# Kernel tuning notes

Hardware: AMD Instinct MI355X
Metric: run time of the kernel (lower is better)

The kernel has to match this reference:

```python
import math
import jax, jax.numpy as jnp
import numpy as np

B, S, H, NH = 4, 2048, 1024, 16
HD = H // NH  # 64


def _rope_cos_sin(seq_len, dim, base=10000.0):
    # freqs[j] = base^(-2j/dim), angles = outer(t, freqs)
    inv = 1.0 / (base ** (jnp.arange(0, dim, 2, dtype=jnp.float32) / dim))
    t = jnp.arange(seq_len, dtype=jnp.float32)
    ang = jnp.outer(t, inv)  # (S, dim//2)
    return jnp.cos(ang), jnp.sin(ang)


def _apply_rope(x, cos, sin):
    # x: (B, S, NH, HD); pairs are (x[2i], x[2i+1]) per torch view_as_complex on reshape(..., -1, 2)
    xr = x.reshape(*x.shape[:-1], HD // 2, 2)
    x0, x1 = xr[..., 0], xr[..., 1]
    c = cos[None, :, None, :]  # (1, S, 1, HD//2)
    s = sin[None, :, None, :]
    o0 = x0 * c - x1 * s
    o1 = x0 * s + x1 * c
    return jnp.stack([o0, o1], axis=-1).reshape(x.shape)


def setup_inputs() -> dict:
    key = jax.random.key(0)
    ks = jax.random.split(key, 5)
    scale = 1.0 / math.sqrt(H)
    return {
        "x": jax.random.normal(ks[0], (B, S, H), dtype=jnp.float32),
        "wq": jax.random.normal(ks[1], (H, H), dtype=jnp.float32) * scale,
        "wk": jax.random.normal(ks[2], (H, H), dtype=jnp.float32) * scale,
        "wv": jax.random.normal(ks[3], (H, H), dtype=jnp.float32) * scale,
        "wo": jax.random.normal(ks[4], (H, H), dtype=jnp.float32) * scale,
        "attention_mask": jnp.ones((B, S), dtype=jnp.int32),
    }


def reference(x, wq, wk, wv, wo, attention_mask):
    # Linear(bias=False): y = x @ W.T with W shape (out, in)
    q = jnp.einsum('bsh,oh->bso', x, wq).reshape(B, S, NH, HD)
    k = jnp.einsum('bsh,oh->bso', x, wk).reshape(B, S, NH, HD)
    v = jnp.einsum('bsh,oh->bso', x, wv).reshape(B, S, NH, HD)
    cos, sin = _rope_cos_sin(S, HD)
    q = _apply_rope(q, cos, sin)
    k = _apply_rope(k, cos, sin)
    # scores: (B, NH, S, S)
    scores = jnp.einsum('bqhd,bkhd->bhqk', q, k) / math.sqrt(HD)
    mask = attention_mask[:, None, None, :]  # (B,1,1,S)
    scores = jnp.where(mask == 0, -jnp.inf, scores)
    attn = jax.nn.softmax(scores, axis=-1)
    # attn_dropout: eval mode / p=0 -> identity
    out = jnp.einsum('bhqk,bkhd->bqhd', attn, v).reshape(B, S, H)
    return jnp.einsum('bsh,oh->bso', out, wo)
```

## Files before the change

kernel.cpp:

```cpp
#include <hip/hip_runtime.h>
#include <hip/hip_bf16.h>

#define B_   4
#define S_   2048
#define H_   1024
#define NH_  16
#define HD_  64
#define M_   8192
#define K_   1024

using bf16x8 = __bf16 __attribute__((ext_vector_type(8)));
using f32x4  = float __attribute__((ext_vector_type(4)));
using f32x16 = float __attribute__((ext_vector_type(16)));

__device__ inline f32x4 mfma16(bf16x8 a, bf16x8 b, f32x4 c) {
    return __builtin_amdgcn_mfma_f32_16x16x32_bf16(a, b, c, 0, 0, 0);
}
__device__ inline f32x16 mfma32(bf16x8 a, bf16x8 b, f32x16 c) {
    return __builtin_amdgcn_mfma_f32_32x32x16_bf16(a, b, c, 0, 0, 0);
}

__device__ inline unsigned short f2bf(float f) {
    __hip_bfloat16 h = __float2bfloat16(f);
    return *reinterpret_cast<unsigned short*>(&h);
}

__device__ inline unsigned cvt_pk_bf16(float lo, float hi) {
    unsigned r;
    asm("v_cvt_pk_bf16_f32 %0, %1, %2" : "=v"(r) : "v"(lo), "v"(hi));
    return r;
}

__device__ inline void perm32swap(unsigned &a, unsigned &b) {
    asm("v_permlane32_swap_b32 %0, %1" : "+v"(a), "+v"(b));
}

__device__ inline void gload_lds16(const unsigned short* g, unsigned short* l) {
    __builtin_amdgcn_global_load_lds(
        (const __attribute__((address_space(1))) void*)g,
        (__attribute__((address_space(3))) void*)l, 16, 0, 0);
}

#define EXP2F(x) __builtin_amdgcn_exp2f(x)


__global__ __launch_bounds__(256) void prep_convert(
    const float* __restrict__ x,  const float* __restrict__ wq,
    const float* __restrict__ wk, const float* __restrict__ wv,
    const float* __restrict__ wo, unsigned short* __restrict__ ws)
{
    size_t u = (size_t)blockIdx.x * 256 + threadIdx.x;
    const float* src; unsigned short* dst; size_t off;
    if (u < 2097152)      { src = x;  dst = ws;            off = u * 4; }
    else if (u < 2359296) { src = wq; dst = ws + 8388608;  off = (u - 2097152) * 4; }
    else if (u < 2621440) { src = wk; dst = ws + 9437184;  off = (u - 2359296) * 4; }
    else if (u < 2883584) { src = wv; dst = ws + 10485760; off = (u - 2621440) * 4; }
    else                  { src = wo; dst = ws + 11534336; off = (u - 2883584) * 4; }
    float4 v = *reinterpret_cast<const float4*>(src + off);
    ushort4 o;
    o.x = f2bf(v.x); o.y = f2bf(v.y); o.z = f2bf(v.z); o.w = f2bf(v.w);
    *reinterpret_cast<ushort4*>(dst + off) = o;
}

__global__ __launch_bounds__(256) void rope_table(
    float* __restrict__ cosb, float* __restrict__ sinb,
    const int* __restrict__ mask, float* __restrict__ biasb)
{
    int idx = blockIdx.x * 256 + threadIdx.x;
    int pos = idx >> 5, i = idx & 31;
    float inv = expf(-(float)(2 * i) * (9.210340371976184f / 64.0f));
    float ang = (float)pos * inv;
    cosb[idx] = cosf(ang);
    sinb[idx] = sinf(ang);
    if (idx < B_ * S_)
        biasb[idx] = mask[idx] ? -12.0f : -__builtin_inff();
}

template<int EPI>
__global__ __launch_bounds__(256) void gemm_bt(
    const unsigned short* __restrict__ A,
    const unsigned short* __restrict__ W,
    void* __restrict__ outp,
    const float* __restrict__ cosb, const float* __restrict__ sinb,
    float scale)
{
    __shared__ alignas(16) unsigned short Al[128 * 64];
    __shared__ alignas(16) unsigned short Bl[128 * 64];

    const int t = threadIdx.x;
    const int l = t & 63;
    const int w = t >> 6;
    const int lane_r = l & 15, lane_g = l >> 4;
    const int bn = blockIdx.x, bm = blockIdx.y;
    const size_t rowbase = (size_t)bm * 128;
    const int colbase = bn * 128;
    const int wm = (w >> 1) * 64, wn = (w & 1) * 64;

    const int glrow  = l >> 3;
    const int glslot = (l & 7) ^ glrow;

    f32x4 zero4 = {0.f, 0.f, 0.f, 0.f};
    f32x4 acc[4][4];
#pragma unroll
    for (int a = 0; a < 4; a++)
#pragma unroll
        for (int b2 = 0; b2 < 4; b2++) acc[a][b2] = zero4;

    for (int k0 = 0; k0 < K_; k0 += 64) {
#pragma unroll
        for (int i = 0; i < 4; i++) {
            int rbase = i * 32 + w * 8;
            int row = rbase + glrow;
            gload_lds16(A + (rowbase + row) * K_ + k0 + glslot * 8, &Al[rbase * 64]);
            gload_lds16(W + (size_t)(colbase + row) * K_ + k0 + glslot * 8, &Bl[rbase * 64]);
        }
        __syncthreads();

        bf16x8 af[4][2], bfr[4][2];
#pragma unroll
        for (int mt = 0; mt < 4; mt++)
#pragma unroll
            for (int kk = 0; kk < 2; kk++) {
                int rowa = wm + mt * 16 + lane_r;
                int offa = (rowa * 128 + kk * 64 + lane_g * 16) ^ ((rowa & 7) << 4);
                af[mt][kk] = *reinterpret_cast<const bf16x8*>((const char*)Al + offa);
                int rowb = wn + mt * 16 + lane_r;
                int offb = (rowb * 128 + kk * 64 + lane_g * 16) ^ ((rowb & 7) << 4);
                bfr[mt][kk] = *reinterpret_cast<const bf16x8*>((const char*)Bl + offb);
            }
#pragma unroll
        for (int mt = 0; mt < 4; mt++)
#pragma unroll
            for (int nt = 0; nt < 4; nt++) {
                acc[mt][nt] = mfma16(af[mt][0], bfr[nt][0], acc[mt][nt]);
                acc[mt][nt] = mfma16(af[mt][1], bfr[nt][1], acc[mt][nt]);
            }
        __syncthreads();
    }

#pragma unroll
    for (int mt = 0; mt < 4; mt++) {
#pragma unroll
        for (int nt = 0; nt < 4; nt++) {
            if constexpr (EPI == 2) {
                float* out = (float*)outp;
#pragma unroll
                for (int i = 0; i < 4; i++) {
                    size_t r = rowbase + wm + mt * 16 + lane_g * 4 + i;
                    int n = colbase + wn + nt * 16 + lane_r;
                    out[r * 1024 + n] = acc[mt][nt][i];
                }
            } else if constexpr (EPI == 0) {
                unsigned short* out = (unsigned short*)outp;
#pragma unroll
                for (int i = 0; i < 4; i++) {
                    size_t r = rowbase + wm + mt * 16 + lane_g * 4 + i;
                    int n = colbase + wn + nt * 16 + lane_r;
                    int b   = (int)(r >> 11);
                    int pos = (int)(r & 2047);
                    int h = n >> 6, d = n & 63;
                    float cv = cosb[pos * 32 + (d >> 1)];
                    float sv = sinb[pos * 32 + (d >> 1)];
                    float val = acc[mt][nt][i];
                    float partner = __shfl_xor(val, 1);
                    float o = (d & 1) ? (partner * sv + val * cv)
                                      : (val * cv - partner * sv);
                    o *= scale;
                    out[(((size_t)(b * NH_ + h)) * S_ + pos) * 64 + d] = f2bf(o);
                }
            } else {
                unsigned short* out = (unsigned short*)outp;
                size_t rr = rowbase + wm + mt * 16 + lane_g * 4;
                int n = colbase + wn + nt * 16 + lane_r;
                int b   = (int)(rr >> 11);
                int pos = (int)(rr & 2047);
                int h = n >> 6, d = n & 63;
                ushort4 o;
                o.x = f2bf(acc[mt][nt][0]); o.y = f2bf(acc[mt][nt][1]);
                o.z = f2bf(acc[mt][nt][2]); o.w = f2bf(acc[mt][nt][3]);
                *reinterpret_cast<ushort4*>(
                    out + (((size_t)(b * NH_ + h)) * 64 + d) * S_ + pos) = o;
            }
        }
    }
}

__global__ __launch_bounds__(256) void attn_fwd(
    const unsigned short* __restrict__ qb, const unsigned short* __restrict__ kb,
    const unsigned short* __restrict__ vt, const float* __restrict__ biasb,
    unsigned short* __restrict__ ao)
{
    __shared__ alignas(16) unsigned short Kl[2][64 * 64];
    __shared__ alignas(16) unsigned short Vl[2][64 * 64];

    const int bid = blockIdx.x;
    const int xcd = bid & 7, idx = bid >> 3;
    const int bh = xcd * 8 + (idx >> 4);
    const int qt = idx & 15;
    const int b = bh >> 4, h = bh & 15;

    const int t = threadIdx.x, l = t & 63, w = t >> 6;
    const int lr = l & 31;
    const int hi = l >> 5;
    const int row8 = lr & 7;

    const unsigned short* qp = qb + (size_t)bh * S_ * 64;
    const unsigned short* kp = kb + (size_t)bh * S_ * 64;
    const unsigned short* vp = vt + (size_t)bh * 64 * S_;
    const float* bp = biasb + (size_t)b * S_;

    bf16x8 qf[4];
    {
        int qrow = qt * 128 + w * 32 + lr;
#pragma unroll
        for (int ks = 0; ks < 4; ks++)
            qf[ks] = *reinterpret_cast<const bf16x8*>(
                qp + (size_t)qrow * 64 + ks * 16 + hi * 8);
    }

    f32x16 oacc[2];
#pragma unroll
    for (int r = 0; r < 16; r++) { oacc[0][r] = 0.f; oacc[1][r] = 0.f; }
    float lsum = 0.f;

    const int grr = l >> 3;
    const int gss = ((l & 7) ^ grr) * 8;

#define STAGE(bi, kt)                                                          \
    {                                                                          \
        _Pragma("unroll")                                                      \
        for (int c = 0; c < 2; c++) {                                          \
            int rbase = w * 16 + c * 8;                                        \
            gload_lds16(kp + (size_t)((kt) * 64 + rbase + grr) * 64 + gss,     \
                        &Kl[bi][rbase * 64]);                                  \
            gload_lds16(vp + (size_t)(rbase + grr) * S_ + (kt) * 64 + gss,     \
                        &Vl[bi][rbase * 64]);                                  \
        }                                                                      \
    }

    STAGE(0, 0)

    for (int kt = 0; kt < 32; kt++) {
        const int cur = kt & 1;
        __syncthreads();
        if (kt < 31) STAGE(cur ^ 1, kt + 1)

        f32x16 sacc[2];
#pragma unroll
        for (int T = 0; T < 2; T++)
#pragma unroll
            for (int g = 0; g < 4; g++) {
                float4 bv = *reinterpret_cast<const float4*>(
                    bp + kt * 64 + T * 32 + g * 8 + hi * 4);
                sacc[T][g * 4 + 0] = bv.x; sacc[T][g * 4 + 1] = bv.y;
                sacc[T][g * 4 + 2] = bv.z; sacc[T][g * 4 + 3] = bv.w;
            }

        __builtin_amdgcn_s_setprio(1);
#pragma unroll
        for (int T = 0; T < 2; T++) {
            int rowb = (32 * T + lr) * 128;
#pragma unroll
            for (int ks = 0; ks < 4; ks++) {
                bf16x8 kf = *reinterpret_cast<const bf16x8*>(
                    (const char*)Kl[cur] + rowb + (((2 * ks + hi) ^ row8) << 4));
                sacc[T] = mfma32(kf, qf[ks], sacc[T]);
            }
        }
        __builtin_amdgcn_s_setprio(0);

        unsigned u[2][8];
        float r0 = 0.f, r1 = 0.f, r2 = 0.f, r3 = 0.f;
#pragma unroll
        for (int T = 0; T < 2; T++) {
            float p[16];
#pragma unroll
            for (int r = 0; r < 16; r++) p[r] = EXP2F(sacc[T][r]);
#pragma unroll
            for (int r = 0; r < 16; r += 4) {
                r0 += p[r]; r1 += p[r + 1]; r2 += p[r + 2]; r3 += p[r + 3];
            }
#pragma unroll
            for (int bq = 0; bq < 4; bq++) {
                u[T][bq * 2 + 0] = cvt_pk_bf16(p[bq * 4 + 0], p[bq * 4 + 1]);
                u[T][bq * 2 + 1] = cvt_pk_bf16(p[bq * 4 + 2], p[bq * 4 + 3]);
            }
        }
        lsum += (r0 + r1) + (r2 + r3);

        bf16x8 pa[4];
#pragma unroll
        for (int ks = 0; ks < 4; ks++) {
            int T = ks >> 1, e = ks & 1;
            unsigned a0 = u[T][4 * e + 0], b0 = u[T][4 * e + 2];
            unsigned a1 = u[T][4 * e + 1], b1 = u[T][4 * e + 3];
            perm32swap(a0, b0);
            perm32swap(a1, b1);
            unsigned q4[4] = {a0, a1, b0, b1};
            pa[ks] = *reinterpret_cast<const bf16x8*>(q4);
        }

        __builtin_amdgcn_s_setprio(1);
#pragma unroll
        for (int dt = 0; dt < 2; dt++) {
            int rowb = (32 * dt + lr) * 128;
#pragma unroll
            for (int ks = 0; ks < 4; ks++) {
                bf16x8 vf = *reinterpret_cast<const bf16x8*>(
                    (const char*)Vl[cur] + rowb + (((2 * ks + hi) ^ row8) << 4));
                oacc[dt] = mfma32(vf, pa[ks], oacc[dt]);
            }
        }
        __builtin_amdgcn_s_setprio(0);
    }
#undef STAGE

    lsum += __shfl_xor(lsum, 32);
    float rl = 1.0f / lsum;
    size_t obase = ((size_t)(b * S_) + qt * 128 + w * 32 + lr) * 1024 + h * 64;
#pragma unroll
    for (int dt = 0; dt < 2; dt++)
#pragma unroll
        for (int g = 0; g < 4; g++) {
            uint2 o;
            o.x = cvt_pk_bf16(oacc[dt][g * 4 + 0] * rl, oacc[dt][g * 4 + 1] * rl);
            o.y = cvt_pk_bf16(oacc[dt][g * 4 + 2] * rl, oacc[dt][g * 4 + 3] * rl);
            *reinterpret_cast<uint2*>(ao + obase + 32 * dt + 8 * g + 4 * hi) = o;
        }
}

extern "C" void kernel_launch(void* const* d_in, const int* in_sizes, int n_in,
                              void* d_out, int out_size, void* d_ws, size_t ws_size,
                              hipStream_t stream)
{
    const float* x  = (const float*)d_in[0];
    const float* wq = (const float*)d_in[1];
    const float* wk = (const float*)d_in[2];
    const float* wv = (const float*)d_in[3];
    const float* wo = (const float*)d_in[4];
    const int* mask = (const int*)d_in[5];

    unsigned short* ws   = (unsigned short*)d_ws;
    unsigned short* xb   = ws;
    unsigned short* wqb  = ws + 8388608;
    unsigned short* wkb  = ws + 9437184;
    unsigned short* wvb  = ws + 10485760;
    unsigned short* wob  = ws + 11534336;
    unsigned short* qbuf = ws + 12582912;
    unsigned short* kbuf = ws + 20971520;
    unsigned short* vtb  = ws + 29360128;
    float* cosb  = (float*)(ws + 37748736);
    float* sinb  = cosb + 65536;
    float* biasb = sinb + 65536;
    unsigned short* aob = xb;

    prep_convert<<<12288, 256, 0, stream>>>(x, wq, wk, wv, wo, ws);
    rope_table<<<256, 256, 0, stream>>>(cosb, sinb, mask, biasb);

    dim3 ggrid(8, 64);
    gemm_bt<0><<<ggrid, 256, 0, stream>>>(xb, wqb, qbuf, cosb, sinb, 0.18033688089184827f);
    gemm_bt<0><<<ggrid, 256, 0, stream>>>(xb, wkb, kbuf, cosb, sinb, 1.0f);
    gemm_bt<1><<<ggrid, 256, 0, stream>>>(xb, wvb, vtb, nullptr, nullptr, 1.0f);

    attn_fwd<<<1024, 256, 0, stream>>>(qbuf, kbuf, vtb, biasb, aob);

    gemm_bt<2><<<ggrid, 256, 0, stream>>>(aob, wob, d_out, nullptr, nullptr, 1.0f);
}
```

Measured before the change: 229.3 us.

## Fuse QKV projections into one GEMM launch and double query rows per attention block

The three Q/K/V projection GEMMs become a single launch over the contiguous concatenated weight buffer, with the output target chosen per column block. The attention kernel now gives each wave two 32-row query sub-tiles that share every K/V tile loaded into LDS, halving the grid and doubling K/V reuse. Register pressure in attention rises (launch bounds set to 2 blocks per SM), and fewer blocks may reduce latency hiding.

```diff
diff --git a/kernel.cpp b/kernel.cpp
--- a/kernel.cpp
+++ b/kernel.cpp
@@ -76,13 +76,12 @@
         biasb[idx] = mask[idx] ? -12.0f : -__builtin_inff();
 }
 
-template<int EPI>
-__global__ __launch_bounds__(256) void gemm_bt(
+__global__ __launch_bounds__(256) void gemm_qkv(
     const unsigned short* __restrict__ A,
     const unsigned short* __restrict__ W,
-    void* __restrict__ outp,
-    const float* __restrict__ cosb, const float* __restrict__ sinb,
-    float scale)
+    unsigned short* __restrict__ qbuf, unsigned short* __restrict__ kbuf,
+    unsigned short* __restrict__ vtb,
+    const float* __restrict__ cosb, const float* __restrict__ sinb)
 {
     __shared__ alignas(16) unsigned short Al[128 * 64];
     __shared__ alignas(16) unsigned short Bl[128 * 64];
@@ -95,6 +94,8 @@
     const size_t rowbase = (size_t)bm * 128;
     const int colbase = bn * 128;
     const int wm = (w >> 1) * 64, wn = (w & 1) * 64;
+    const int which = colbase >> 10;
+    const float scale = (which == 0) ? 0.18033688089184827f : 1.0f;
 
     const int glrow  = l >> 3;
     const int glslot = (l & 7) ^ glrow;
@@ -142,20 +143,12 @@
     for (int mt = 0; mt < 4; mt++) {
 #pragma unroll
         for (int nt = 0; nt < 4; nt++) {
-            if constexpr (EPI == 2) {
-                float* out = (float*)outp;
+            if (which <= 1) {
+                unsigned short* out = which ? kbuf : qbuf;
 #pragma unroll
                 for (int i = 0; i < 4; i++) {
                     size_t r = rowbase + wm + mt * 16 + lane_g * 4 + i;
-                    int n = colbase + wn + nt * 16 + lane_r;
-                    out[r * 1024 + n] = acc[mt][nt][i];
-                }
-            } else if constexpr (EPI == 0) {
-                unsigned short* out = (unsigned short*)outp;
-#pragma unroll
-                for (int i = 0; i < 4; i++) {
-                    size_t r = rowbase + wm + mt * 16 + lane_g * 4 + i;
-                    int n = colbase + wn + nt * 16 + lane_r;
+                    int n = (colbase & 1023) + wn + nt * 16 + lane_r;
                     int b   = (int)(r >> 11);
                     int pos = (int)(r & 2047);
                     int h = n >> 6, d = n & 63;
@@ -169,9 +162,9 @@
                     out[(((size_t)(b * NH_ + h)) * S_ + pos) * 64 + d] = f2bf(o);
                 }
             } else {
-                unsigned short* out = (unsigned short*)outp;
+                unsigned short* out = vtb;
                 size_t rr = rowbase + wm + mt * 16 + lane_g * 4;
-                int n = colbase + wn + nt * 16 + lane_r;
+                int n = (colbase & 1023) + wn + nt * 16 + lane_r;
                 int b   = (int)(rr >> 11);
                 int pos = (int)(rr & 2047);
                 int h = n >> 6, d = n & 63;
@@ -185,7 +178,78 @@
     }
 }
 
-__global__ __launch_bounds__(256) void attn_fwd(
+__global__ __launch_bounds__(256) void gemm_wo(
+    const unsigned short* __restrict__ A,
+    const unsigned short* __restrict__ W,
+    float* __restrict__ out)
+{
+    __shared__ alignas(16) unsigned short Al[128 * 64];
+    __shared__ alignas(16) unsigned short Bl[128 * 64];
+
+    const int t = threadIdx.x;
+    const int l = t & 63;
+    const int w = t >> 6;
+    const int lane_r = l & 15, lane_g = l >> 4;
+    const int bn = blockIdx.x, bm = blockIdx.y;
+    const size_t rowbase = (size_t)bm * 128;
+    const int colbase = bn * 128;
+    const int wm = (w >> 1) * 64, wn = (w & 1) * 64;
+
+    const int glrow  = l >> 3;
+    const int glslot = (l & 7) ^ glrow;
+
+    f32x4 zero4 = {0.f, 0.f, 0.f, 0.f};
+    f32x4 acc[4][4];
+#pragma unroll
+    for (int a = 0; a < 4; a++)
+#pragma unroll
+        for (int b2 = 0; b2 < 4; b2++) acc[a][b2] = zero4;
+
+    for (int k0 = 0; k0 < K_; k0 += 64) {
+#pragma unroll
+        for (int i = 0; i < 4; i++) {
+            int rbase = i * 32 + w * 8;
+            int row = rbase + glrow;
+            gload_lds16(A + (rowbase + row) * K_ + k0 + glslot * 8, &Al[rbase * 64]);
+            gload_lds16(W + (size_t)(colbase + row) * K_ + k0 + glslot * 8, &Bl[rbase * 64]);
+        }
+        __syncthreads();
+
+        bf16x8 af[4][2], bfr[4][2];
+#pragma unroll
+        for (int mt = 0; mt < 4; mt++)
+#pragma unroll
+            for (int kk = 0; kk < 2; kk++) {
+                int rowa = wm + mt * 16 + lane_r;
+                int offa = (rowa * 128 + kk * 64 + lane_g * 16) ^ ((rowa & 7) << 4);
+                af[mt][kk] = *reinterpret_cast<const bf16x8*>((const char*)Al + offa);
+                int rowb = wn + mt * 16 + lane_r;
+                int offb = (rowb * 128 + kk * 64 + lane_g * 16) ^ ((rowb & 7) << 4);
+                bfr[mt][kk] = *reinterpret_cast<const bf16x8*>((const char*)Bl + offb);
+            }
+#pragma unroll
+        for (int mt = 0; mt < 4; mt++)
+#pragma unroll
+            for (int nt = 0; nt < 4; nt++) {
+                acc[mt][nt] = mfma16(af[mt][0], bfr[nt][0], acc[mt][nt]);
+                acc[mt][nt] = mfma16(af[mt][1], bfr[nt][1], acc[mt][nt]);
+            }
+        __syncthreads();
+    }
+
+#pragma unroll
+    for (int mt = 0; mt < 4; mt++)
+#pragma unroll
+        for (int nt = 0; nt < 4; nt++)
+#pragma unroll
+            for (int i = 0; i < 4; i++) {
+                size_t r = rowbase + wm + mt * 16 + lane_g * 4 + i;
+                int n = colbase + wn + nt * 16 + lane_r;
+                out[r * 1024 + n] = acc[mt][nt][i];
+            }
+}
+
+__global__ __launch_bounds__(256, 2) void attn_fwd(
     const unsigned short* __restrict__ qb, const unsigned short* __restrict__ kb,
     const unsigned short* __restrict__ vt, const float* __restrict__ biasb,
     unsigned short* __restrict__ ao)
@@ -195,8 +259,8 @@
 
     const int bid = blockIdx.x;
     const int xcd = bid & 7, idx = bid >> 3;
-    const int bh = xcd * 8 + (idx >> 4);
-    const int qt = idx & 15;
+    const int bh = xcd * 8 + (idx >> 3);
+    const int qt = idx & 7;
     const int b = bh >> 4, h = bh & 15;
 
     const int t = threadIdx.x, l = t & 63, w = t >> 6;
@@ -209,19 +273,22 @@
     const unsigned short* vp = vt + (size_t)bh * 64 * S_;
     const float* bp = biasb + (size_t)b * S_;
 
-    bf16x8 qf[4];
-    {
-        int qrow = qt * 128 + w * 32 + lr;
+    bf16x8 qf[2][4];
+#pragma unroll
+    for (int qbk = 0; qbk < 2; qbk++) {
+        int qrow = qt * 256 + w * 64 + qbk * 32 + lr;
 #pragma unroll
         for (int ks = 0; ks < 4; ks++)
-            qf[ks] = *reinterpret_cast<const bf16x8*>(
+            qf[qbk][ks] = *reinterpret_cast<const bf16x8*>(
                 qp + (size_t)qrow * 64 + ks * 16 + hi * 8);
     }
 
-    f32x16 oacc[2];
-#pragma unroll
-    for (int r = 0; r < 16; r++) { oacc[0][r] = 0.f; oacc[1][r] = 0.f; }
-    float lsum = 0.f;
+    f32x16 oacc[2][2];
+#pragma unroll
+    for (int qbk = 0; qbk < 2; qbk++)
+#pragma unroll
+        for (int r = 0; r < 16; r++) { oacc[qbk][0][r] = 0.f; oacc[qbk][1][r] = 0.f; }
+    float lsum[2] = {0.f, 0.f};
 
     const int grr = l >> 3;
     const int gss = ((l & 7) ^ grr) * 8;
@@ -245,16 +312,18 @@
         __syncthreads();
         if (kt < 31) STAGE(cur ^ 1, kt + 1)
 
-        f32x16 sacc[2];
-#pragma unroll
-        for (int T = 0; T < 2; T++)
+        f32x16 sacc[2][2];
+#pragma unroll
+        for (int T = 0; T < 2; T++) {
 #pragma unroll
             for (int g = 0; g < 4; g++) {
                 float4 bv = *reinterpret_cast<const float4*>(
                     bp + kt * 64 + T * 32 + g * 8 + hi * 4);
-                sacc[T][g * 4 + 0] = bv.x; sacc[T][g * 4 + 1] = bv.y;
-                sacc[T][g * 4 + 2] = bv.z; sacc[T][g * 4 + 3] = bv.w;
-            }
+                sacc[0][T][g * 4 + 0] = bv.x; sacc[0][T][g * 4 + 1] = bv.y;
+                sacc[0][T][g * 4 + 2] = bv.z; sacc[0][T][g * 4 + 3] = bv.w;
+            }
+            sacc[1][T] = sacc[0][T];
+        }
 
         __builtin_amdgcn_s_setprio(1);
 #pragma unroll
@@ -264,40 +333,43 @@
             for (int ks = 0; ks < 4; ks++) {
                 bf16x8 kf = *reinterpret_cast<const bf16x8*>(
                     (const char*)Kl[cur] + rowb + (((2 * ks + hi) ^ row8) << 4));
-                sacc[T] = mfma32(kf, qf[ks], sacc[T]);
+                sacc[0][T] = mfma32(kf, qf[0][ks], sacc[0][T]);
+                sacc[1][T] = mfma32(kf, qf[1][ks], sacc[1][T]);
             }
         }
         __builtin_amdgcn_s_setprio(0);
 
-        unsigned u[2][8];
-        float r0 = 0.f, r1 = 0.f, r2 = 0.f, r3 = 0.f;
-#pragma unroll
-        for (int T = 0; T < 2; T++) {
-            float p[16];
-#pragma unroll
-            for (int r = 0; r < 16; r++) p[r] = EXP2F(sacc[T][r]);
-#pragma unroll
-            for (int r = 0; r < 16; r += 4) {
-                r0 += p[r]; r1 += p[r + 1]; r2 += p[r + 2]; r3 += p[r + 3];
-            }
-#pragma unroll
-            for (int bq = 0; bq < 4; bq++) {
-                u[T][bq * 2 + 0] = cvt_pk_bf16(p[bq * 4 + 0], p[bq * 4 + 1]);
-                u[T][bq * 2 + 1] = cvt_pk_bf16(p[bq * 4 + 2], p[bq * 4 + 3]);
-            }
-        }
-        lsum += (r0 + r1) + (r2 + r3);
-
-        bf16x8 pa[4];
-#pragma unroll
-        for (int ks = 0; ks < 4; ks++) {
-            int T = ks >> 1, e = ks & 1;
-            unsigned a0 = u[T][4 * e + 0], b0 = u[T][4 * e + 2];
-            unsigned a1 = u[T][4 * e + 1], b1 = u[T][4 * e + 3];
-            perm32swap(a0, b0);
-            perm32swap(a1, b1);
-            unsigned q4[4] = {a0, a1, b0, b1};
-            pa[ks] = *reinterpret_cast<const bf16x8*>(q4);
+        bf16x8 pa[2][4];
+#pragma unroll
+        for (int qbk = 0; qbk < 2; qbk++) {
+            unsigned u[2][8];
+            float r0 = 0.f, r1 = 0.f, r2 = 0.f, r3 = 0.f;
+#pragma unroll
+            for (int T = 0; T < 2; T++) {
+                float p[16];
+#pragma unroll
+                for (int r = 0; r < 16; r++) p[r] = EXP2F(sacc[qbk][T][r]);
+#pragma unroll
+                for (int r = 0; r < 16; r += 4) {
+                    r0 += p[r]; r1 += p[r + 1]; r2 += p[r + 2]; r3 += p[r + 3];
+                }
+#pragma unroll
+                for (int bq = 0; bq < 4; bq++) {
+                    u[T][bq * 2 + 0] = cvt_pk_bf16(p[bq * 4 + 0], p[bq * 4 + 1]);
+                    u[T][bq * 2 + 1] = cvt_pk_bf16(p[bq * 4 + 2], p[bq * 4 + 3]);
+                }
+            }
+            lsum[qbk] += (r0 + r1) + (r2 + r3);
+#pragma unroll
+            for (int ks = 0; ks < 4; ks++) {
+                int T = ks >> 1, e = ks & 1;
+                unsigned a0 = u[T][4 * e + 0], b0 = u[T][4 * e + 2];
+                unsigned a1 = u[T][4 * e + 1], b1 = u[T][4 * e + 3];
+                perm32swap(a0, b0);
+                perm32swap(a1, b1);
+                unsigned q4[4] = {a0, a1, b0, b1};
+                pa[qbk][ks] = *reinterpret_cast<const bf16x8*>(q4);
+            }
         }
 
         __builtin_amdgcn_s_setprio(1);
@@ -308,25 +380,30 @@
             for (int ks = 0; ks < 4; ks++) {
                 bf16x8 vf = *reinterpret_cast<const bf16x8*>(
                     (const char*)Vl[cur] + rowb + (((2 * ks + hi) ^ row8) << 4));
-                oacc[dt] = mfma32(vf, pa[ks], oacc[dt]);
+                oacc[0][dt] = mfma32(vf, pa[0][ks], oacc[0][dt]);
+                oacc[1][dt] = mfma32(vf, pa[1][ks], oacc[1][dt]);
             }
         }
         __builtin_amdgcn_s_setprio(0);
     }
 #undef STAGE
 
-    lsum += __shfl_xor(lsum, 32);
-    float rl = 1.0f / lsum;
-    size_t obase = ((size_t)(b * S_) + qt * 128 + w * 32 + lr) * 1024 + h * 64;
-#pragma unroll
-    for (int dt = 0; dt < 2; dt++)
-#pragma unroll
-        for (int g = 0; g < 4; g++) {
-            uint2 o;
-            o.x = cvt_pk_bf16(oacc[dt][g * 4 + 0] * rl, oacc[dt][g * 4 + 1] * rl);
-            o.y = cvt_pk_bf16(oacc[dt][g * 4 + 2] * rl, oacc[dt][g * 4 + 3] * rl);
-            *reinterpret_cast<uint2*>(ao + obase + 32 * dt + 8 * g + 4 * hi) = o;
-        }
+#pragma unroll
+    for (int qbk = 0; qbk < 2; qbk++) {
+        float ls = lsum[qbk];
+        ls += __shfl_xor(ls, 32);
+        float rl = 1.0f / ls;
+        size_t obase = ((size_t)(b * S_) + qt * 256 + w * 64 + qbk * 32 + lr) * 1024 + h * 64;
+#pragma unroll
+        for (int dt = 0; dt < 2; dt++)
+#pragma unroll
+            for (int g = 0; g < 4; g++) {
+                uint2 o;
+                o.x = cvt_pk_bf16(oacc[qbk][dt][g * 4 + 0] * rl, oacc[qbk][dt][g * 4 + 1] * rl);
+                o.y = cvt_pk_bf16(oacc[qbk][dt][g * 4 + 2] * rl, oacc[qbk][dt][g * 4 + 3] * rl);
+                *reinterpret_cast<uint2*>(ao + obase + 32 * dt + 8 * g + 4 * hi) = o;
+            }
+    }
 }
 
 extern "C" void kernel_launch(void* const* d_in, const int* in_sizes, int n_in,
@@ -342,9 +419,7 @@
 
     unsigned short* ws   = (unsigned short*)d_ws;
     unsigned short* xb   = ws;
-    unsigned short* wqb  = ws + 8388608;
-    unsigned short* wkb  = ws + 9437184;
-    unsigned short* wvb  = ws + 10485760;
+    unsigned short* wqkv = ws + 8388608;
     unsigned short* wob  = ws + 11534336;
     unsigned short* qbuf = ws + 12582912;
     unsigned short* kbuf = ws + 20971520;
@@ -357,12 +432,9 @@
     prep_convert<<<12288, 256, 0, stream>>>(x, wq, wk, wv, wo, ws);
     rope_table<<<256, 256, 0, stream>>>(cosb, sinb, mask, biasb);
 
-    dim3 ggrid(8, 64);
-    gemm_bt<0><<<ggrid, 256, 0, stream>>>(xb, wqb, qbuf, cosb, sinb, 0.18033688089184827f);
-    gemm_bt<0><<<ggrid, 256, 0, stream>>>(xb, wkb, kbuf, cosb, sinb, 1.0f);
-    gemm_bt<1><<<ggrid, 256, 0, stream>>>(xb, wvb, vtb, nullptr, nullptr, 1.0f);
-
-    attn_fwd<<<1024, 256, 0, stream>>>(qbuf, kbuf, vtb, biasb, aob);
-
-    gemm_bt<2><<<ggrid, 256, 0, stream>>>(aob, wob, d_out, nullptr, nullptr, 1.0f);
-}
+    gemm_qkv<<<dim3(24, 64), 256, 0, stream>>>(xb, wqkv, qbuf, kbuf, vtb, cosb, sinb);
+
+    attn_fwd<<<512, 256, 0, stream>>>(qbuf, kbuf, vtb, biasb, aob);
+
+    gemm_wo<<<dim3(8, 64), 256, 0, stream>>>(aob, wob, (float*)d_out);
+}
```

Result: faster. 203.7 us (-11.2%).
